# Kernel tuning notes

Measured on AMD Instinct MI355X. Metric: run time of the kernel, lower is better.

The kernel has to match this reference:

```python
import jax, jax.numpy as jnp
import numpy as np


def setup_inputs() -> dict:
    key = jax.random.key(0)
    ks = jax.random.split(key, 7)
    T, B, X, H = 256, 64, 512, 2048
    s_ih = 1.0 / np.sqrt(H)
    return {
        "input": jax.random.normal(ks[0], (T, B, X), dtype=jnp.float32),
        "h_0": jax.random.normal(ks[1], (B, H), dtype=jnp.float32),
        "c_0": jax.random.normal(ks[2], (B, H), dtype=jnp.float32),
        "w_ih": jax.random.normal(ks[3], (4 * H, X), dtype=jnp.float32) * s_ih,
        "w_hh": jax.random.normal(ks[4], (4 * H, H), dtype=jnp.float32) * s_ih,
        "b_ih": jax.random.normal(ks[5], (4 * H,), dtype=jnp.float32) * s_ih,
        "b_hh": jax.random.normal(ks[6], (4 * H,), dtype=jnp.float32) * s_ih,
    }


def reference(input, h_0, c_0, w_ih, w_hh, b_ih, b_hh):
    H = h_0.shape[-1]
    # Precompute input projections for all timesteps in one big GEMM: [T,B,4H]
    x_proj = jnp.einsum("tbx,gx->tbg", input, w_ih) + b_ih + b_hh

    def step(carry, xg):
        h, c = carry
        gates = xg + h @ w_hh.T  # [B, 4H]
        i, f, g, o = jnp.split(gates, 4, axis=-1)  # torch LSTMCell gate order
        i = jax.nn.sigmoid(i)
        f = jax.nn.sigmoid(f)
        g = jnp.tanh(g)
        o = jax.nn.sigmoid(o)
        c_new = f * c + i * g
        h_new = o * jnp.tanh(c_new)
        y = jax.nn.softmax(h_new, axis=-1)  # per-step softmax over hidden dim
        return (h_new, c_new), y

    (h_T, c_T), ys = jax.lax.scan(step, (h_0, c_0), x_proj)
    return ys, h_T, c_T
```

## Files before the change

kernel.cpp:

```cpp
#include <hip/hip_runtime.h>

#define Tn 256
#define Bn 64
#define Xn 512
#define Hn 2048
#define Gn 8192
#define NWG 256

typedef short bf16x8 __attribute__((ext_vector_type(8)));
typedef float f32x4 __attribute__((ext_vector_type(4)));
typedef unsigned uint32x4 __attribute__((ext_vector_type(4)));

#define AL(p)    __hip_atomic_load((p), __ATOMIC_RELAXED, __HIP_MEMORY_SCOPE_AGENT)
#define AS(p, v) __hip_atomic_store((p), (v), __ATOMIC_RELAXED, __HIP_MEMORY_SCOPE_AGENT)
#define AADD(p, v) __hip_atomic_fetch_add((p), (v), __ATOMIC_RELAXED, __HIP_MEMORY_SCOPE_AGENT)

static __device__ __forceinline__ unsigned short f2bf(float f) {
    unsigned int u = __builtin_bit_cast(unsigned int, f);
    u += 0x7fffu + ((u >> 16) & 1u);
    return (unsigned short)(u >> 16);
}
static __device__ __forceinline__ float bf2f(unsigned short s) {
    unsigned int u = ((unsigned int)s) << 16;
    return __builtin_bit_cast(float, u);
}
static __device__ __forceinline__ void cvt4(const float* __restrict__ s,
                                            unsigned short* __restrict__ d, int i) {
    float4 v = ((const float4*)s)[i];
    ushort4 o;
    o.x = f2bf(v.x); o.y = f2bf(v.y); o.z = f2bf(v.z); o.w = f2bf(v.w);
    ((ushort4*)d)[i] = o;
}
static __device__ __forceinline__ float sigm(float x) {
    return 1.f / (1.f + __expf(-x));
}
static __device__ __forceinline__ float ftanh(float x) {
    float e = __expf(2.f * x);
    return (e - 1.f) / (e + 1.f);
}

template <int RING>
static __device__ __forceinline__ size_t hoff(int t) {
    if constexpr (RING) return (size_t)((t * 97) % 257) * 262144;
    else                return (size_t)(t & 1) * 262144;
}
template <int RING>
static __device__ __forceinline__ bf16x8 ldh(const unsigned short* p) {
    if constexpr (RING) {
        return *(const bf16x8*)p;
    } else {
        unsigned* q = (unsigned*)p;
        uint32x4 v;
        v[0] = AL(q + 0); v[1] = AL(q + 1); v[2] = AL(q + 2); v[3] = AL(q + 3);
        return __builtin_bit_cast(bf16x8, v);
    }
}
template <int RING>
static __device__ __forceinline__ float ldh1(const unsigned short* hb, int idx) {
    if constexpr (RING) {
        return bf2f(hb[idx]);
    } else {
        unsigned d = AL((unsigned*)(hb + (idx & ~1)));
        return bf2f((idx & 1) ? (unsigned short)(d >> 16) : (unsigned short)(d & 0xffffu));
    }
}

static __device__ __forceinline__ void shards_wait(unsigned* sh, unsigned t, int l) {
    if (!t) return;
    const unsigned target = t * 32u;
    const bool mine = (l < 8);
    for (;;) {
        unsigned a = mine ? AL(sh + l) : target;
        if (__all(a >= target)) break;
        __builtin_amdgcn_s_sleep(1);
    }
}

__global__ void prologue3(const float* __restrict__ x, const float* __restrict__ h0,
                          const float* __restrict__ b_ih, const float* __restrict__ b_hh,
                          const float* __restrict__ w_ih,
                          unsigned short* __restrict__ Xb, unsigned short* __restrict__ XFrag,
                          unsigned short* __restrict__ hb0, float* __restrict__ bias,
                          unsigned* __restrict__ flags)
{
    int i = blockIdx.x * blockDim.x + threadIdx.x;
    const int n_x  = Tn * Bn * Xn / 4;
    const int n_xf = Gn * Xn / 4;
    const int n_h  = Bn * Hn / 4;
    const int n_b  = Gn / 4;
    if (i < n_x) { cvt4(x, Xb, i); return; }
    i -= n_x;
    if (i < n_xf) {
        int wg = i >> 12, r = i & 4095;
        int c = r >> 7, k = (r & 127) * 4;
        int g = c >> 3, u = c & 7;
        float4 v = *(const float4*)(w_ih + (size_t)(g * Hn + wg * 8 + u) * Xn + k);
        ushort4 o;
        o.x = f2bf(v.x); o.y = f2bf(v.y); o.z = f2bf(v.z); o.w = f2bf(v.w);
        int ct = c >> 4, kk = k >> 5, l = ((k >> 3) & 3) * 16 + (c & 15);
        *(ushort4*)((char*)XFrag + (size_t)wg * 32768 + (size_t)((ct * 16 + kk) * 64 + l) * 16 + (k & 7) * 2) = o;
        return;
    }
    i -= n_xf;
    if (i < n_h) {
        int flat = i * 4;
        int row = flat >> 11, unit0 = flat & 2047;
        float4 v = ((const float4*)h0)[i];
        ushort4 o;
        o.x = f2bf(v.x); o.y = f2bf(v.y); o.z = f2bf(v.z); o.w = f2bf(v.w);
        int dst = (((unit0 >> 3) << 6) + row) * 8 + (unit0 & 7);
        *(ushort4*)(hb0 + dst) = o;
        return;
    }
    i -= n_h;
    if (i < n_b) {
        float4 a = ((const float4*)b_ih)[i];
        float4 b = ((const float4*)b_hh)[i];
        ((float4*)bias)[i] = make_float4(a.x + b.x, a.y + b.y, a.z + b.z, a.w + b.w);
        return;
    }
    i -= n_b;
    if (i < 256) flags[i] = 0u;
}

#define MFMA4(a0v, a1v) \
    acc00 = __builtin_amdgcn_mfma_f32_16x16x32_bf16((a0v), b0, acc00, 0, 0, 0); \
    acc10 = __builtin_amdgcn_mfma_f32_16x16x32_bf16((a1v), b0, acc10, 0, 0, 0); \
    acc01 = __builtin_amdgcn_mfma_f32_16x16x32_bf16((a0v), b1, acc01, 0, 0, 0); \
    acc11 = __builtin_amdgcn_mfma_f32_16x16x32_bf16((a1v), b1, acc11, 0, 0, 0);

template <int RING>
__global__ __launch_bounds__(512, 2) void lstm_persist4(
    const unsigned short* __restrict__ Xb, const unsigned short* __restrict__ XFrag,
    const float* __restrict__ bias, const float* __restrict__ c0,
    char* __restrict__ hbase, const float* __restrict__ w_hh,
    float* __restrict__ ys, float* __restrict__ hT, float* __restrict__ cT,
    unsigned* __restrict__ shards)
{
    extern __shared__ char smem[];
    const unsigned short* LW = (const unsigned short*)smem;
    float* RED  = (float*)(smem + 131072);
    float* RED2 = (float*)(smem + 155648);

    const int wg  = blockIdx.x;
    const int tid = threadIdx.x;
    const int U0  = wg * 8;

    for (int i = tid; i < 32 * 512; i += 512) {
        int c = i >> 9, k = (i & 511) * 4;
        int g = c >> 3, u = c & 7;
        float4 v = *(const float4*)(w_hh + (size_t)(g * Hn + U0 + u) * Hn + k);
        ushort4 o;
        o.x = f2bf(v.x); o.y = f2bf(v.y); o.z = f2bf(v.z); o.w = f2bf(v.w);
        int ct = c >> 4, kk = k >> 5, l = ((k >> 3) & 3) * 16 + (c & 15);
        *(ushort4*)(smem + ((size_t)((ct * 64 + kk) * 64 + l) * 16 + (k & 7) * 2)) = o;
    }
    __syncthreads();

    const int w = tid >> 6, l = tid & 63;
    const int lm = l & 15, lh = l >> 4;
    const int kh = w >> 1, rblk = w & 1, rb = rblk * 32;
    const int kk0 = kh * 16;
    const int kx0 = kh * 4;

    const int u  = lm & 7;
    const bool hi = (lm & 8) != 0;

    float bi = 0.f, bf_ = 0.f, bg = 0.f, bo = 0.f;
    float cs[2][2] = {{0.f, 0.f}, {0.f, 0.f}};
    if (kh == 0) {
        bi  = bias[0 * Hn + U0 + u];
        bf_ = bias[1 * Hn + U0 + u];
        bg  = bias[2 * Hn + U0 + u];
        bo  = bias[3 * Hn + U0 + u];
        #pragma unroll
        for (int s = 0; s < 2; ++s)
            #pragma unroll
            for (int j = 0; j < 2; ++j)
                cs[s][j] = c0[(size_t)(rb + s * 16 + 4 * lh + (hi ? 2 : 0) + j) * Hn + U0 + u];
    }

    const char* xfb = (const char*)XFrag + (size_t)wg * 32768;
    const int srb = w - 2;

    for (int t = 0; t < Tn; ++t) {
        const unsigned short* hb = (const unsigned short*)(hbase + hoff<RING>(t));
        unsigned short* hn = (unsigned short*)(hbase + hoff<RING>(t + 1));

        f32x4 acc00 = {0,0,0,0}, acc01 = {0,0,0,0}, acc10 = {0,0,0,0}, acc11 = {0,0,0,0};

        {
            const unsigned short* xa0 = Xb + (size_t)(t * 64 + rb + lm) * Xn + lh * 8;
            const unsigned short* xa1 = xa0 + 16 * Xn;
            bf16x8 xA0[4], xA1[4];
            #pragma unroll
            for (int j = 0; j < 4; ++j) {
                xA0[j] = *(const bf16x8*)(xa0 + (kx0 + j) * 32);
                xA1[j] = *(const bf16x8*)(xa1 + (kx0 + j) * 32);
            }
            #pragma unroll
            for (int kkl = 0; kkl < 4; ++kkl) {
                bf16x8 b0 = *(const bf16x8*)(xfb + ((size_t)((0 * 16 + kx0 + kkl) * 64 + l) << 4));
                bf16x8 b1 = *(const bf16x8*)(xfb + ((size_t)((1 * 16 + kx0 + kkl) * 64 + l) << 4));
                MFMA4(xA0[kkl], xA1[kkl]);
            }
        }

        if (w == 0) shards_wait(shards, (unsigned)t, l);
        __syncthreads();

        {
            const unsigned short* ha0 = hb + (size_t)(rb + lm) * 8;
            const unsigned short* ha1 = ha0 + 128;
            bf16x8 aP0[4], aP1[4];
            #pragma unroll
            for (int j = 0; j < 4; ++j) {
                int g = (kk0 + j) * 4 + lh;
                aP0[j] = ldh<RING>(ha0 + (size_t)g * 512);
                aP1[j] = ldh<RING>(ha1 + (size_t)g * 512);
            }
            #pragma unroll 4
            for (int kkl = 0; kkl < 16; ++kkl) {
                bf16x8 a0v = aP0[kkl & 3], a1v = aP1[kkl & 3];
                if (kkl < 12) {
                    int g = (kk0 + kkl + 4) * 4 + lh;
                    aP0[kkl & 3] = ldh<RING>(ha0 + (size_t)g * 512);
                    aP1[kkl & 3] = ldh<RING>(ha1 + (size_t)g * 512);
                }
                bf16x8 b0 = *(const bf16x8*)(LW + ((size_t)((0 * 64 + kk0 + kkl) * 64 + l) << 3));
                bf16x8 b1 = *(const bf16x8*)(LW + ((size_t)((1 * 64 + kk0 + kkl) * 64 + l) << 3));
                MFMA4(a0v, a1v);
            }
        }

        const bool do_sm = (srb >= 0 && srb < 4) && (wg < Bn) && (t > 0);
        float sv[8];
        if (kh != 0) {
            int idx = (((kh - 1) * 2 + rblk) * 64 + l) * 16;
            *(f32x4*)(RED + idx + 0)  = acc00;
            *(f32x4*)(RED + idx + 4)  = acc01;
            *(f32x4*)(RED + idx + 8)  = acc10;
            *(f32x4*)(RED + idx + 12) = acc11;
            if (do_sm) {
                int row = wg;
                float m = -1e30f;
                #pragma unroll
                for (int j = 0; j < 8; ++j) {
                    int uu = srb * 512 + j * 64 + l;
                    sv[j] = ldh1<RING>(hb, (uu >> 3) * 512 + row * 8 + (uu & 7));
                    m = fmaxf(m, sv[j]);
                }
                #pragma unroll
                for (int off = 32; off; off >>= 1) m = fmaxf(m, __shfl_xor(m, off));
                float s = 0.f;
                #pragma unroll
                for (int j = 0; j < 8; ++j) s += __expf(sv[j] - m);
                #pragma unroll
                for (int off = 32; off; off >>= 1) s += __shfl_xor(s, off);
                if (l == 0) { RED2[srb * 2] = m; RED2[srb * 2 + 1] = s; }
            }
        }
        __syncthreads();

        if (kh == 0) {
            #pragma unroll
            for (int p = 0; p < 3; ++p) {
                int idx = ((p * 2 + rblk) * 64 + l) * 16;
                acc00 += *(const f32x4*)(RED + idx + 0);
                acc01 += *(const f32x4*)(RED + idx + 4);
                acc10 += *(const f32x4*)(RED + idx + 8);
                acc11 += *(const f32x4*)(RED + idx + 12);
            }
            f32x4 sA[2], sB[2];
            #pragma unroll
            for (int r = 0; r < 4; ++r) {
                sA[0][r] = __shfl_xor(acc00[r], 8); sB[0][r] = __shfl_xor(acc01[r], 8);
                sA[1][r] = __shfl_xor(acc10[r], 8); sB[1][r] = __shfl_xor(acc11[r], 8);
            }
            #pragma unroll
            for (int s = 0; s < 2; ++s) {
                f32x4 aA = s ? acc10 : acc00;
                f32x4 aB = s ? acc11 : acc01;
                #pragma unroll
                for (int j = 0; j < 2; ++j) {
                    int r = (hi ? 2 : 0) + j;
                    float gi = (hi ? sA[s][r] : aA[r]) + bi;
                    float gf = (hi ? aA[r] : sA[s][r]) + bf_;
                    float gg = (hi ? sB[s][r] : aB[r]) + bg;
                    float go = (hi ? aB[r] : sB[s][r]) + bo;
                    float iv = sigm(gi), fv = sigm(gf), gv = ftanh(gg), ov = sigm(go);
                    float cc = cs[s][j];
                    float cn = fv * cc + iv * gv;
                    float hv = ov * ftanh(cn);
                    cs[s][j] = cn;
                    int rowg = rb + s * 16 + 4 * lh + (hi ? 2 : 0) + j;
                    unsigned short mybf = f2bf(hv);
                    unsigned other = (unsigned)__shfl_xor((int)(unsigned)mybf, 1);
                    if (!(u & 1)) {
                        AS((unsigned*)(hn + (size_t)wg * 512 + rowg * 8 + u),
                           (unsigned)mybf | (other << 16));
                    }
                    if (t == Tn - 1) {
                        size_t off = (size_t)rowg * Hn + U0 + u;
                        hT[off] = hv;
                        cT[off] = cn;
                    }
                }
            }
        }
        __syncthreads();
        if (tid == 0) AADD(shards + (wg >> 5), 1u);

        if (do_sm) {
            float m0 = RED2[0], sA0 = RED2[1], m1 = RED2[2], sB0 = RED2[3];
            float m2 = RED2[4], sC0 = RED2[5], m3 = RED2[6], sD0 = RED2[7];
            float gm = fmaxf(fmaxf(m0, m1), fmaxf(m2, m3));
            float gs = sA0 * __expf(m0 - gm) + sB0 * __expf(m1 - gm) +
                       sC0 * __expf(m2 - gm) + sD0 * __expf(m3 - gm);
            float inv = 1.f / gs;
            float* yr = ys + ((size_t)(t - 1) * Bn + wg) * Hn + srb * 512;
            #pragma unroll
            for (int j = 0; j < 8; ++j) yr[j * 64 + l] = __expf(sv[j] - gm) * inv;
        }
    }

    if (w == 0) shards_wait(shards, (unsigned)Tn, l);
    __syncthreads();
    {
        const unsigned short* hfin = (const unsigned short*)(hbase + hoff<RING>(Tn));
        const bool act = (srb >= 0 && srb < 4) && (wg < Bn);
        float sv[8];
        if (act) {
            int row = wg;
            float m = -1e30f;
            #pragma unroll
            for (int j = 0; j < 8; ++j) {
                int uu = srb * 512 + j * 64 + l;
                sv[j] = ldh1<RING>(hfin, (uu >> 3) * 512 + row * 8 + (uu & 7));
                m = fmaxf(m, sv[j]);
            }
            #pragma unroll
            for (int off = 32; off; off >>= 1) m = fmaxf(m, __shfl_xor(m, off));
            float s = 0.f;
            #pragma unroll
            for (int j = 0; j < 8; ++j) s += __expf(sv[j] - m);
            #pragma unroll
            for (int off = 32; off; off >>= 1) s += __shfl_xor(s, off);
            if (l == 0) { RED2[srb * 2] = m; RED2[srb * 2 + 1] = s; }
        }
        __syncthreads();
        if (act) {
            float m0 = RED2[0], sA0 = RED2[1], m1 = RED2[2], sB0 = RED2[3];
            float m2 = RED2[4], sC0 = RED2[5], m3 = RED2[6], sD0 = RED2[7];
            float gm = fmaxf(fmaxf(m0, m1), fmaxf(m2, m3));
            float gs = sA0 * __expf(m0 - gm) + sB0 * __expf(m1 - gm) +
                       sC0 * __expf(m2 - gm) + sD0 * __expf(m3 - gm);
            float inv = 1.f / gs;
            float* yr = ys + ((size_t)(Tn - 1) * Bn + wg) * Hn + srb * 512;
            #pragma unroll
            for (int j = 0; j < 8; ++j) yr[j * 64 + l] = __expf(sv[j] - gm) * inv;
        }
    }
}

extern "C" void kernel_launch(void* const* d_in, const int* in_sizes, int n_in,
                              void* d_out, int out_size, void* d_ws, size_t ws_size,
                              hipStream_t stream) {
    const float* input = (const float*)d_in[0];
    const float* h0    = (const float*)d_in[1];
    const float* c0    = (const float*)d_in[2];
    const float* w_ih  = (const float*)d_in[3];
    const float* w_hh  = (const float*)d_in[4];
    const float* b_ih  = (const float*)d_in[5];
    const float* b_hh  = (const float*)d_in[6];

    float* ys = (float*)d_out;
    float* hT = ys + (size_t)Tn * Bn * Hn;
    float* cT = hT + (size_t)Bn * Hn;

    char* wsb = (char*)d_ws;
    unsigned short* Xb  = (unsigned short*)wsb;
    unsigned short* XF  = (unsigned short*)(wsb + 16777216);
    float* bias         = (float*)(wsb + 25165824);
    unsigned* flags     = (unsigned*)(wsb + 25198592);
    char* hbase         = wsb + 25199616;
    const size_t need_ring = 25199616 + (size_t)257 * 262144;

    const int prol_items = Tn * Bn * Xn / 4 + Gn * Xn / 4 + Bn * Hn / 4 + Gn / 4 + 256;
    const int prol_blocks = (prol_items + 255) / 256;
    prologue3<<<dim3(prol_blocks), dim3(256), 0, stream>>>(
        input, h0, b_ih, b_hh, w_ih, Xb, XF, (unsigned short*)hbase, bias, flags);

    if (ws_size >= need_ring) {
        (void)hipFuncSetAttribute((const void*)lstm_persist4<1>,
                                  hipFuncAttributeMaxDynamicSharedMemorySize, 155680);
        lstm_persist4<1><<<dim3(NWG), dim3(512), 155680, stream>>>(
            Xb, XF, bias, c0, hbase, w_hh, ys, hT, cT, flags);
    } else {
        (void)hipFuncSetAttribute((const void*)lstm_persist4<0>,
                                  hipFuncAttributeMaxDynamicSharedMemorySize, 155680);
        lstm_persist4<0><<<dim3(NWG), dim3(512), 155680, stream>>>(
            Xb, XF, bias, c0, hbase, w_hh, ys, hT, cT, flags);
    }
}
```

Measured before the change: 2.160 ms.

## Replace global shard barrier with per-wave pair waits on padded counters

Each wave now waits only on the two shard counters covering the slice of h it reads, rather than wave 0 polling all eight shards and then hitting a workgroup barrier. The shard counters are padded to 16-word stride so they sit in separate cache lines, and the partial-sum scratch layout is regrouped into per-accumulator planes. The goal is to let waves start their recurrent GEMM as soon as their own dependencies are ready and to cut contention on the shared counters. In exchange, many more waves poll global memory, and the flags region must be large enough for the padded stride (prologue zeroes 256 words, which is enough).

New measurement: 1.958 ms. -9.4%, faster.

```diff
diff --git a/kernel.cpp b/kernel.cpp
--- a/kernel.cpp
+++ b/kernel.cpp
@@ -65,12 +65,12 @@
     }
 }
 
-static __device__ __forceinline__ void shards_wait(unsigned* sh, unsigned t, int l) {
-    if (!t) return;
-    const unsigned target = t * 32u;
-    const bool mine = (l < 8);
+static __device__ __forceinline__ void pair_wait(unsigned* sh, int s0, int s1,
+                                                 unsigned target, int l) {
+    if (!target) return;
+    unsigned* p = sh + ((l == 0) ? s0 : s1) * 16;
     for (;;) {
-        unsigned a = mine ? AL(sh + l) : target;
+        unsigned a = AL(p);
         if (__all(a >= target)) break;
         __builtin_amdgcn_s_sleep(1);
     }
@@ -130,7 +130,7 @@
     acc11 = __builtin_amdgcn_mfma_f32_16x16x32_bf16((a1v), b1, acc11, 0, 0, 0);
 
 template <int RING>
-__global__ __launch_bounds__(512, 2) void lstm_persist4(
+__global__ __launch_bounds__(512, 2) void lstm_persist5(
     const unsigned short* __restrict__ Xb, const unsigned short* __restrict__ XFrag,
     const float* __restrict__ bias, const float* __restrict__ c0,
     char* __restrict__ hbase, const float* __restrict__ w_hh,
@@ -163,7 +163,7 @@
     const int kk0 = kh * 16;
     const int kx0 = kh * 4;
 
-    const int u  = lm & 7;
+    const int u  = lm & 15 & 7;
     const bool hi = (lm & 8) != 0;
 
     float bi = 0.f, bf_ = 0.f, bg = 0.f, bo = 0.f;
@@ -206,8 +206,7 @@
             }
         }
 
-        if (w == 0) shards_wait(shards, (unsigned)t, l);
-        __syncthreads();
+        pair_wait(shards, 2 * kh, 2 * kh + 1, (unsigned)t * 32u, l);
 
         {
             const unsigned short* ha0 = hb + (size_t)(rb + lm) * 8;
@@ -236,12 +235,14 @@
         const bool do_sm = (srb >= 0 && srb < 4) && (wg < Bn) && (t > 0);
         float sv[8];
         if (kh != 0) {
-            int idx = (((kh - 1) * 2 + rblk) * 64 + l) * 16;
-            *(f32x4*)(RED + idx + 0)  = acc00;
-            *(f32x4*)(RED + idx + 4)  = acc01;
-            *(f32x4*)(RED + idx + 8)  = acc10;
-            *(f32x4*)(RED + idx + 12) = acc11;
+            int slot = (kh - 1) * 2 + rblk;
+            int base = (slot * 64 + l) * 4;
+            *(f32x4*)(RED + 0 * 1536 + base) = acc00;
+            *(f32x4*)(RED + 1 * 1536 + base) = acc01;
+            *(f32x4*)(RED + 2 * 1536 + base) = acc10;
+            *(f32x4*)(RED + 3 * 1536 + base) = acc11;
             if (do_sm) {
+                pair_wait(shards, 2 * srb, 2 * srb + 1, (unsigned)t * 32u, l);
                 int row = wg;
                 float m = -1e30f;
                 #pragma unroll
@@ -265,11 +266,11 @@
         if (kh == 0) {
             #pragma unroll
             for (int p = 0; p < 3; ++p) {
-                int idx = ((p * 2 + rblk) * 64 + l) * 16;
-                acc00 += *(const f32x4*)(RED + idx + 0);
-                acc01 += *(const f32x4*)(RED + idx + 4);
-                acc10 += *(const f32x4*)(RED + idx + 8);
-                acc11 += *(const f32x4*)(RED + idx + 12);
+                int base = ((p * 2 + rblk) * 64 + l) * 4;
+                acc00 += *(const f32x4*)(RED + 0 * 1536 + base);
+                acc01 += *(const f32x4*)(RED + 1 * 1536 + base);
+                acc10 += *(const f32x4*)(RED + 2 * 1536 + base);
+                acc11 += *(const f32x4*)(RED + 3 * 1536 + base);
             }
             f32x4 sA[2], sB[2];
             #pragma unroll
@@ -309,7 +310,7 @@
             }
         }
         __syncthreads();
-        if (tid == 0) AADD(shards + (wg >> 5), 1u);
+        if (tid == 0) AADD(shards + (wg >> 5) * 16, 1u);
 
         if (do_sm) {
             float m0 = RED2[0], sA0 = RED2[1], m1 = RED2[2], sB0 = RED2[3];
@@ -324,13 +325,12 @@
         }
     }
 
-    if (w == 0) shards_wait(shards, (unsigned)Tn, l);
-    __syncthreads();
     {
         const unsigned short* hfin = (const unsigned short*)(hbase + hoff<RING>(Tn));
         const bool act = (srb >= 0 && srb < 4) && (wg < Bn);
         float sv[8];
         if (act) {
+            pair_wait(shards, 2 * srb, 2 * srb + 1, (unsigned)Tn * 32u, l);
             int row = wg;
             float m = -1e30f;
             #pragma unroll
@@ -392,14 +392,14 @@
         input, h0, b_ih, b_hh, w_ih, Xb, XF, (unsigned short*)hbase, bias, flags);
 
     if (ws_size >= need_ring) {
-        (void)hipFuncSetAttribute((const void*)lstm_persist4<1>,
+        (void)hipFuncSetAttribute((const void*)lstm_persist5<1>,
                                   hipFuncAttributeMaxDynamicSharedMemorySize, 155680);
-        lstm_persist4<1><<<dim3(NWG), dim3(512), 155680, stream>>>(
+        lstm_persist5<1><<<dim3(NWG), dim3(512), 155680, stream>>>(
             Xb, XF, bias, c0, hbase, w_hh, ys, hT, cT, flags);
     } else {
-        (void)hipFuncSetAttribute((const void*)lstm_persist4<0>,
+        (void)hipFuncSetAttribute((const void*)lstm_persist5<0>,
                                   hipFuncAttributeMaxDynamicSharedMemorySize, 155680);
-        lstm_persist4<0><<<dim3(NWG), dim3(512), 155680, stream>>>(
+        lstm_persist5<0><<<dim3(NWG), dim3(512), 155680, stream>>>(
             Xb, XF, bias, c0, hbase, w_hh, ys, hT, cT, flags);
     }
 }
```
